# Kernel optimization log

Measured on AMD Instinct MI355X. Metric: run time of the kernel, lower is better.

The kernel has to match this reference:

```python
import jax, jax.numpy as jnp
import numpy as np

SIGMA = 0.01        # config['fscore_sigma']
FSCORE_W = 0.1      # config['fscore_weight']
TASK_W = 1.0        # config['task_weight']
DOMAIN_W = 0.1      # config['domain_weight']


def setup_inputs() -> dict:
    key = jax.random.key(0)
    ks = jax.random.split(key, 11)
    B, N, M, F = 8, 4096, 4096, 512
    H1, H2, D = 256, 128, 6
    return {
        "pred_pc": jax.random.normal(ks[0], (B, N, 3), jnp.float32),
        "target_pc": jax.random.normal(ks[1], (B, M, 3), jnp.float32),
        "domain_features": jax.random.normal(ks[2], (B, F), jnp.float32),
        "dataset_weights": jax.random.uniform(ks[3], (B,), jnp.float32, 0.9, 1.2),
        "W1": jax.random.normal(ks[4], (F, H1), jnp.float32) * 0.02,
        "b1": jnp.zeros((H1,), jnp.float32),
        "W2": jax.random.normal(ks[5], (H1, H2), jnp.float32) * 0.02,
        "b2": jnp.zeros((H2,), jnp.float32),
        "W3": jax.random.normal(ks[6], (H2, D), jnp.float32) * 0.02,
        "b3": jnp.zeros((D,), jnp.float32),
        "domain_labels": jax.random.randint(ks[7], (B,), 0, D),
    }


def _chamfer_mins(pred, tgt):
    # pred: [B,N,3], tgt: [B,M,3] -> squared pairwise dists [B,N,M], then dual mins
    d = (jnp.sum(pred ** 2, axis=2)[:, :, None]
         + jnp.sum(tgt ** 2, axis=2)[:, None, :]
         - 2.0 * jnp.einsum('bnd,bmd->bnm', pred, tgt))
    return jnp.min(d, axis=2), jnp.min(d, axis=1)   # [B,N], [B,M]


def reference(pred_pc, target_pc, domain_features, dataset_weights,
              W1, b1, W2, b2, W3, b3, domain_labels):
    min_a, min_b = _chamfer_mins(pred_pc, target_pc)
    c = 2.0 * SIGMA * SIGMA
    soft_a = jnp.exp(-min_a / c)
    soft_b = jnp.exp(-min_b / c)

    # batch-level task loss (compute_reconstruction_loss on full batch)
    chamfer = jnp.mean(min_a) + jnp.mean(min_b)
    prec = jnp.mean(soft_a)
    rec = jnp.mean(soft_b)
    fscore = 2.0 * prec * rec / (prec + rec + 1e-8)
    task = chamfer + FSCORE_W * (1.0 - fscore)

    # per-sample dataset-weighted loss (vectorized form of the Python loop)
    ch_i = jnp.mean(min_a, axis=1) + jnp.mean(min_b, axis=1)
    p_i = jnp.mean(soft_a, axis=1)
    r_i = jnp.mean(soft_b, axis=1)
    f_i = 2.0 * p_i * r_i / (p_i + r_i + 1e-8)
    loss_i = ch_i + FSCORE_W * (1.0 - f_i)
    dataset_weighted = jnp.mean(dataset_weights * loss_i)

    # domain loss: GRL is identity in forward; classifier in eval mode (dropout off)
    h = jax.nn.relu(domain_features @ W1 + b1)
    h = jax.nn.relu(h @ W2 + b2)
    logits = h @ W3 + b3
    logp = jax.nn.log_softmax(logits, axis=-1)
    domain = -jnp.mean(jnp.take_along_axis(logp, domain_labels[:, None], axis=1))

    total = TASK_W * task + DOMAIN_W * domain + dataset_weighted
    return total
```

## Files before the change

### kernel.cpp

```cpp
#include <hip/hip_runtime.h>
#include <math.h>

#define B 8
#define NPTS 4096
#define QPT 8
#define THREADS 256


template<int S, int LOG2S>
__global__ __launch_bounds__(THREADS, 4) void d1_kernel(
    const float* __restrict__ pred, const float* __restrict__ targ,
    const float* __restrict__ x, const float* __restrict__ W1,
    float* __restrict__ partial, float* __restrict__ sums32,
    float* __restrict__ h1p) {
  constexpr int REFS = NPTS / S;
  int id = blockIdx.x;
  int tid = threadIdx.x;

  __shared__ float4 refs[REFS];
  __shared__ float xs[64];

  if (id < 64) {
    if (id == 0 && tid < 32) sums32[tid] = 0.f;
    int b = id >> 3, kc = id & 7;
    if (tid < 64) xs[tid] = x[b * 512 + kc * 64 + tid];
    __syncthreads();
    float acc = 0.f;
    const float* w = W1 + (size_t)(kc * 64) * 256 + tid;
#pragma unroll 8
    for (int k = 0; k < 64; ++k) acc = fmaf(xs[k], w[k * 256], acc);
    h1p[(b * 8 + kc) * 256 + tid] = acc;
    return;
  }

  int cid = id - 64;
  int split  = cid & (S - 1);
  int qchunk = (cid >> LOG2S) & 1;
  int b      = (cid >> (LOG2S + 1)) & 7;
  int dir    = cid >> (LOG2S + 4);
  const float* qp = dir ? targ : pred;
  const float* rp = dir ? pred : targ;

  const float* rb = rp + ((size_t)b * NPTS + (size_t)split * REFS) * 3;
  for (int i = tid; i < REFS; i += THREADS) {
    float xx = rb[i * 3 + 0], yy = rb[i * 3 + 1], zz = rb[i * 3 + 2];
    refs[i] = make_float4(xx, yy, zz, 0.5f * (xx * xx + yy * yy + zz * zz));
  }
  __syncthreads();

  const float* qb = qp + (size_t)b * NPTS * 3;
  int q0 = qchunk * (QPT * THREADS) + tid;
  float qx[QPT], qy[QPT], qz[QPT], vmin[QPT];
#pragma unroll
  for (int i = 0; i < QPT; ++i) {
    int q = q0 + i * THREADS;
    qx[i] = qb[q * 3 + 0];
    qy[i] = qb[q * 3 + 1];
    qz[i] = qb[q * 3 + 2];
    vmin[i] = 3.4e38f;
  }

  for (int j = 0; j < REFS; j += 8) {
    float4 t[8];
#pragma unroll
    for (int u = 0; u < 8; ++u) t[u] = refs[j + u];
#pragma unroll
    for (int i = 0; i < QPT; ++i) {
      float s[8];
#pragma unroll
      for (int u = 0; u < 8; ++u)
        s[u] = fmaf(-qx[i], t[u].x,
               fmaf(-qy[i], t[u].y, fmaf(-qz[i], t[u].z, t[u].w)));
      float m01 = fminf(s[0], s[1]), m23 = fminf(s[2], s[3]);
      float m45 = fminf(s[4], s[5]), m67 = fminf(s[6], s[7]);
      vmin[i] = fminf(vmin[i],
                      fminf(fminf(m01, m23), fminf(m45, m67)));
    }
  }

  size_t base = (((size_t)dir * B + b) * S + split) * NPTS;
#pragma unroll
  for (int i = 0; i < QPT; ++i) {
    float qn = fmaf(qx[i], qx[i], fmaf(qy[i], qy[i], qz[i] * qz[i]));
    partial[base + q0 + i * THREADS] = fmaf(2.f, vmin[i], qn);
  }
}

template<int S>
__global__ __launch_bounds__(THREADS) void d2_kernel(
    const float* __restrict__ partial, float* __restrict__ sums32,
    const float* __restrict__ h1p, const float* __restrict__ b1,
    const float* __restrict__ W2, float* __restrict__ h2p) {
  int id = blockIdx.x;
  int tid = threadIdx.x;

  if (id >= 256) {
    int lid = id - 256;
    int b = lid >> 1, half = lid & 1;
    __shared__ float hs[128];
    if (tid < 128) {
      int k = half * 128 + tid;
      float a = b1[k];
#pragma unroll
      for (int p = 0; p < 8; ++p) a += h1p[(b * 8 + p) * 256 + k];
      hs[tid] = fmaxf(a, 0.f);
    }
    __syncthreads();
    if (tid < 128) {
      float acc = 0.f;
      const float* w = W2 + (size_t)(half * 128) * 128 + tid;
#pragma unroll 8
      for (int k = 0; k < 128; ++k) acc = fmaf(hs[k], w[k * 128], acc);
      h2p[(b * 2 + half) * 128 + tid] = acc;
    }
    return;
  }

  int chunk = id & 15;
  int b   = (id >> 4) & 7;
  int dir = id >> 7;
  size_t pb = ((size_t)dir * B + b) * S * NPTS;
  int q = chunk * 256 + tid;

  float m = 3.4e38f;
#pragma unroll
  for (int s = 0; s < S; ++s)
    m = fminf(m, partial[pb + (size_t)s * NPTS + q]);
  float s_min = m;
  float s_soft = __expf(-5000.0f * m);

  for (int off = 32; off > 0; off >>= 1) {
    s_min  += __shfl_down(s_min,  off);
    s_soft += __shfl_down(s_soft, off);
  }
  __shared__ float red[8];
  int wave = tid >> 6, lane = tid & 63;
  if (lane == 0) { red[wave * 2] = s_min; red[wave * 2 + 1] = s_soft; }
  __syncthreads();
  if (tid == 0) {
    float a = 0.f, c = 0.f;
    for (int w = 0; w < 4; ++w) { a += red[w * 2]; c += red[w * 2 + 1]; }
    atomicAdd(&sums32[(dir * B + b) * 2 + 0], a);
    atomicAdd(&sums32[(dir * B + b) * 2 + 1], c);
  }
}

__global__ __launch_bounds__(THREADS) void final_kernel(
    const float* __restrict__ h2p, const float* __restrict__ b2,
    const float* __restrict__ W3, const float* __restrict__ b3,
    const int* __restrict__ labels, const float* __restrict__ sums32,
    const float* __restrict__ w, float* __restrict__ out) {
  int tid = threadIdx.x;
  __shared__ float h2s[8 * 128];
  __shared__ float lg[48];
  __shared__ float nlls[8];

  for (int i = tid; i < 1024; i += THREADS) {
    int b = i >> 7, j = i & 127;
    float a = b2[j] + h2p[(b * 2 + 0) * 128 + j] + h2p[(b * 2 + 1) * 128 + j];
    h2s[i] = fmaxf(a, 0.f);
  }
  __syncthreads();
  if (tid < 48) {
    int b = tid / 6, d = tid % 6;
    float acc = b3[d];
#pragma unroll 8
    for (int k = 0; k < 128; ++k) acc = fmaf(h2s[b * 128 + k], W3[k * 6 + d], acc);
    lg[tid] = acc;
  }
  __syncthreads();
  if (tid < 8) {
    int b = tid;
    float mx = lg[b * 6];
    for (int d = 1; d < 6; ++d) mx = fmaxf(mx, lg[b * 6 + d]);
    float se = 0.f;
    for (int d = 0; d < 6; ++d) se += __expf(lg[b * 6 + d] - mx);
    int lab = labels[b];
    nlls[b] = -(lg[b * 6 + lab] - mx - __logf(se));
  }
  __syncthreads();
  if (tid == 0) {
    float chamfer = 0.f, prec = 0.f, rec = 0.f, dsw = 0.f, dom = 0.f;
    for (int b = 0; b < B; ++b) {
      float sa  = sums32[(0 * B + b) * 2 + 0];
      float ssa = sums32[(0 * B + b) * 2 + 1];
      float sb  = sums32[(1 * B + b) * 2 + 0];
      float ssb = sums32[(1 * B + b) * 2 + 1];
      float ma = sa / 4096.f, mb = sb / 4096.f;
      float p = ssa / 4096.f, r = ssb / 4096.f;
      chamfer += ma + mb;
      prec += p; rec += r;
      float f_i = 2.f * p * r / (p + r + 1e-8f);
      float loss_i = ma + mb + 0.1f * (1.f - f_i);
      dsw += w[b] * loss_i;
      dom += nlls[b];
    }
    chamfer *= (1.f / B); prec *= (1.f / B); rec *= (1.f / B);
    dsw *= (1.f / B); dom *= (1.f / B);
    float fscore = 2.f * prec * rec / (prec + rec + 1e-8f);
    float task = chamfer + 0.1f * (1.f - fscore);
    out[0] = 1.0f * task + 0.1f * dom + dsw;
  }
}

template<int S, int LOG2S>
static void run_pipeline(const float* pred, const float* targ, const float* x,
                         const float* wgt, const float* W1, const float* b1,
                         const float* W2, const float* b2, const float* W3,
                         const float* b3, const int* labels, float* out,
                         char* ws, hipStream_t stream) {
  float* partial = (float*)ws;
  float* sums32  = partial + (size_t)2 * B * S * NPTS;
  float* h1p     = sums32 + 32;
  float* h2p     = h1p + 64 * 256;

  hipLaunchKernelGGL((d1_kernel<S, LOG2S>), dim3(64 + 32 * S), dim3(THREADS),
                     0, stream, pred, targ, x, W1, partial, sums32, h1p);
  hipLaunchKernelGGL((d2_kernel<S>), dim3(256 + 16), dim3(THREADS), 0, stream,
                     partial, sums32, h1p, b1, W2, h2p);
  hipLaunchKernelGGL(final_kernel, dim3(1), dim3(THREADS), 0, stream,
                     h2p, b2, W3, b3, labels, sums32, wgt, out);
}

extern "C" void kernel_launch(void* const* d_in, const int* in_sizes, int n_in,
                              void* d_out, int out_size, void* d_ws, size_t ws_size,
                              hipStream_t stream) {
  const float* pred   = (const float*)d_in[0];
  const float* targ   = (const float*)d_in[1];
  const float* x      = (const float*)d_in[2];
  const float* wgt    = (const float*)d_in[3];
  const float* W1     = (const float*)d_in[4];
  const float* b1     = (const float*)d_in[5];
  const float* W2     = (const float*)d_in[6];
  const float* b2     = (const float*)d_in[7];
  const float* W3     = (const float*)d_in[8];
  const float* b3     = (const float*)d_in[9];
  const int*   labels = (const int*)d_in[10];
  float* out = (float*)d_out;
  char* ws = (char*)d_ws;

  auto need = [](int S) {
    return ((size_t)2 * B * S * NPTS + 32 + 64 * 256 + 16 * 128) * sizeof(float);
  };
  if (ws_size >= need(32))
    run_pipeline<32, 5>(pred, targ, x, wgt, W1, b1, W2, b2, W3, b3, labels,
                        out, ws, stream);
  else if (ws_size >= need(16))
    run_pipeline<16, 4>(pred, targ, x, wgt, W1, b1, W2, b2, W3, b3, labels,
                        out, ws, stream);
  else
    run_pipeline<8, 3>(pred, targ, x, wgt, W1, b1, W2, b2, W3, b3, labels,
                       out, ws, stream);
}
```

Measured before the change: 112.6 us.

## Fuse chamfer reduction and MLP tail into one kernel via last-block atomics

```diff
diff --git a/kernel.cpp b/kernel.cpp
--- a/kernel.cpp
+++ b/kernel.cpp
@@ -7,200 +7,224 @@
 #define THREADS 256
 
 
+__device__ __forceinline__ void final_combine(
+    const float* sums32, const float* nlls, const float* w, float* out) {
+  float chamfer = 0.f, prec = 0.f, rec = 0.f, dsw = 0.f, dom = 0.f;
+  for (int b = 0; b < B; ++b) {
+    float sa  = sums32[(0 * B + b) * 2 + 0];
+    float ssa = sums32[(0 * B + b) * 2 + 1];
+    float sb  = sums32[(1 * B + b) * 2 + 0];
+    float ssb = sums32[(1 * B + b) * 2 + 1];
+    float ma = sa / 4096.f, mb = sb / 4096.f;
+    float p = ssa / 4096.f, r = ssb / 4096.f;
+    chamfer += ma + mb;
+    prec += p; rec += r;
+    float f_i = 2.f * p * r / (p + r + 1e-8f);
+    float loss_i = ma + mb + 0.1f * (1.f - f_i);
+    dsw += w[b] * loss_i;
+    dom += nlls[b];
+  }
+  chamfer *= (1.f / B); prec *= (1.f / B); rec *= (1.f / B);
+  dsw *= (1.f / B); dom *= (1.f / B);
+  float fscore = 2.f * prec * rec / (prec + rec + 1e-8f);
+  float task = chamfer + 0.1f * (1.f - fscore);
+  out[0] = 1.0f * task + 0.1f * dom + dsw;
+}
+
+__global__ __launch_bounds__(THREADS) void k_init_l1(
+    const float* __restrict__ x, const float* __restrict__ W1,
+    float* __restrict__ h1p, float* __restrict__ sums32,
+    unsigned int* __restrict__ cnt) {
+  int id = blockIdx.x, tid = threadIdx.x;
+  if (id == 0) {
+    if (tid < 32) sums32[tid] = 0.f;
+    if (tid < 33) cnt[tid] = 0u;
+  }
+  int b = id >> 3, kc = id & 7;
+  __shared__ float xs[64];
+  if (tid < 64) xs[tid] = x[b * 512 + kc * 64 + tid];
+  __syncthreads();
+  float acc = 0.f;
+  const float* w = W1 + (size_t)(kc * 64) * 256 + tid;
+#pragma unroll 8
+  for (int k = 0; k < 64; ++k) acc = fmaf(xs[k], w[k * 256], acc);
+  h1p[(b * 8 + kc) * 256 + tid] = acc;
+}
+
 template<int S, int LOG2S>
-__global__ __launch_bounds__(THREADS, 4) void d1_kernel(
+__global__ __launch_bounds__(THREADS, 4) void k_fused(
     const float* __restrict__ pred, const float* __restrict__ targ,
-    const float* __restrict__ x, const float* __restrict__ W1,
+    const float* __restrict__ h1p, const float* __restrict__ b1,
+    const float* __restrict__ W2, const float* __restrict__ b2,
+    const float* __restrict__ W3, const float* __restrict__ b3,
+    const int* __restrict__ labels, const float* __restrict__ wgt,
     float* __restrict__ partial, float* __restrict__ sums32,
-    float* __restrict__ h1p) {
+    float* __restrict__ nlls, unsigned int* __restrict__ cnt,
+    float* __restrict__ out) {
   constexpr int REFS = NPTS / S;
-  int id = blockIdx.x;
-  int tid = threadIdx.x;
-
-  __shared__ float4 refs[REFS];
-  __shared__ float xs[64];
-
-  if (id < 64) {
-    if (id == 0 && tid < 32) sums32[tid] = 0.f;
-    int b = id >> 3, kc = id & 7;
-    if (tid < 64) xs[tid] = x[b * 512 + kc * 64 + tid];
-    __syncthreads();
-    float acc = 0.f;
-    const float* w = W1 + (size_t)(kc * 64) * 256 + tid;
-#pragma unroll 8
-    for (int k = 0; k < 64; ++k) acc = fmaf(xs[k], w[k * 256], acc);
-    h1p[(b * 8 + kc) * 256 + tid] = acc;
+  int id = blockIdx.x, tid = threadIdx.x;
+
+  __shared__ float4 sbuf4[1040];
+  float* sbuf = (float*)sbuf4;
+  __shared__ unsigned int sflag;
+
+  if (id < 32 * S) {
+    int cid = id;
+    int split  = cid & (S - 1);
+    int qchunk = (cid >> LOG2S) & 1;
+    int b      = (cid >> (LOG2S + 1)) & 7;
+    int dir    = cid >> (LOG2S + 4);
+    const float* qp = dir ? targ : pred;
+    const float* rp = dir ? pred : targ;
+
+    float4* refs = sbuf4;
+    const float* rb = rp + ((size_t)b * NPTS + (size_t)split * REFS) * 3;
+    for (int i = tid; i < REFS; i += THREADS) {
+      float xx = rb[i * 3 + 0], yy = rb[i * 3 + 1], zz = rb[i * 3 + 2];
+      refs[i] = make_float4(xx, yy, zz, 0.5f * (xx * xx + yy * yy + zz * zz));
+    }
+    __syncthreads();
+
+    const float* qb = qp + (size_t)b * NPTS * 3;
+    int q0 = qchunk * (QPT * THREADS) + tid;
+    float qx[QPT], qy[QPT], qz[QPT], vmin[QPT];
+#pragma unroll
+    for (int i = 0; i < QPT; ++i) {
+      int q = q0 + i * THREADS;
+      qx[i] = qb[q * 3 + 0];
+      qy[i] = qb[q * 3 + 1];
+      qz[i] = qb[q * 3 + 2];
+      vmin[i] = 3.4e38f;
+    }
+
+    for (int j = 0; j < REFS; j += 4) {
+      float4 t0 = refs[j + 0], t1 = refs[j + 1];
+      float4 t2 = refs[j + 2], t3 = refs[j + 3];
+      asm volatile("" : "+v"(t0.x), "+v"(t0.y), "+v"(t0.z), "+v"(t0.w),
+                        "+v"(t1.x), "+v"(t1.y), "+v"(t1.z), "+v"(t1.w),
+                        "+v"(t2.x), "+v"(t2.y), "+v"(t2.z), "+v"(t2.w),
+                        "+v"(t3.x), "+v"(t3.y), "+v"(t3.z), "+v"(t3.w));
+#pragma unroll
+      for (int i = 0; i < QPT; ++i) {
+        float s0 = fmaf(-qx[i], t0.x, fmaf(-qy[i], t0.y, fmaf(-qz[i], t0.z, t0.w)));
+        float s1 = fmaf(-qx[i], t1.x, fmaf(-qy[i], t1.y, fmaf(-qz[i], t1.z, t1.w)));
+        float s2 = fmaf(-qx[i], t2.x, fmaf(-qy[i], t2.y, fmaf(-qz[i], t2.z, t2.w)));
+        float s3 = fmaf(-qx[i], t3.x, fmaf(-qy[i], t3.y, fmaf(-qz[i], t3.z, t3.w)));
+        vmin[i] = fminf(fminf(vmin[i], fminf(s0, s1)), fminf(s2, s3));
+      }
+    }
+
+    size_t base = (((size_t)dir * B + b) * S + split) * NPTS;
+#pragma unroll
+    for (int i = 0; i < QPT; ++i) {
+      float qn = fmaf(qx[i], qx[i], fmaf(qy[i], qy[i], qz[i] * qz[i]));
+      partial[base + q0 + i * THREADS] = fmaf(2.f, vmin[i], qn);
+    }
+
+    __threadfence();
+    if (tid == 0) {
+      unsigned int old = atomicAdd(&cnt[(dir * 8 + b) * 2 + qchunk], 1u);
+      sflag = (old == (unsigned int)(S - 1)) ? 1u : 0u;
+    }
+    __syncthreads();
+    if (!sflag) return;
+
+    __threadfence();
+    size_t pb = (size_t)(dir * B + b) * S * NPTS;
+    float s_min = 0.f, s_soft = 0.f;
+#pragma unroll
+    for (int u = 0; u < QPT; ++u) {
+      int q = qchunk * (QPT * THREADS) + u * THREADS + tid;
+      float m = 3.4e38f;
+      for (int s = 0; s < S; ++s)
+        m = fminf(m, partial[pb + (size_t)s * NPTS + q]);
+      s_min  += m;
+      s_soft += __expf(-5000.0f * m);
+    }
+    for (int off = 32; off > 0; off >>= 1) {
+      s_min  += __shfl_down(s_min,  off);
+      s_soft += __shfl_down(s_soft, off);
+    }
+    int wave = tid >> 6, lane = tid & 63;
+    float* red = sbuf + 4160;
+    if (lane == 0) { red[wave * 2] = s_min; red[wave * 2 + 1] = s_soft; }
+    __syncthreads();
+    if (tid == 0) {
+      float a = 0.f, c = 0.f;
+      for (int w = 0; w < 4; ++w) { a += red[w * 2]; c += red[w * 2 + 1]; }
+      atomicAdd(&sums32[(dir * B + b) * 2 + 0], a);
+      atomicAdd(&sums32[(dir * B + b) * 2 + 1], c);
+      __threadfence();
+      unsigned int old = atomicAdd(&cnt[32], 1u);
+      sflag = (old == 32u) ? 1u : 0u;
+    }
+    __syncthreads();
+    if (sflag && tid == 0) { __threadfence(); final_combine(sums32, nlls, wgt, out); }
     return;
   }
 
-  int cid = id - 64;
-  int split  = cid & (S - 1);
-  int qchunk = (cid >> LOG2S) & 1;
-  int b      = (cid >> (LOG2S + 1)) & 7;
-  int dir    = cid >> (LOG2S + 4);
-  const float* qp = dir ? targ : pred;
-  const float* rp = dir ? pred : targ;
-
-  const float* rb = rp + ((size_t)b * NPTS + (size_t)split * REFS) * 3;
-  for (int i = tid; i < REFS; i += THREADS) {
-    float xx = rb[i * 3 + 0], yy = rb[i * 3 + 1], zz = rb[i * 3 + 2];
-    refs[i] = make_float4(xx, yy, zz, 0.5f * (xx * xx + yy * yy + zz * zz));
-  }
-  __syncthreads();
-
-  const float* qb = qp + (size_t)b * NPTS * 3;
-  int q0 = qchunk * (QPT * THREADS) + tid;
-  float qx[QPT], qy[QPT], qz[QPT], vmin[QPT];
-#pragma unroll
-  for (int i = 0; i < QPT; ++i) {
-    int q = q0 + i * THREADS;
-    qx[i] = qb[q * 3 + 0];
-    qy[i] = qb[q * 3 + 1];
-    qz[i] = qb[q * 3 + 2];
-    vmin[i] = 3.4e38f;
-  }
-
-  for (int j = 0; j < REFS; j += 8) {
-    float4 t[8];
-#pragma unroll
-    for (int u = 0; u < 8; ++u) t[u] = refs[j + u];
-#pragma unroll
-    for (int i = 0; i < QPT; ++i) {
-      float s[8];
-#pragma unroll
-      for (int u = 0; u < 8; ++u)
-        s[u] = fmaf(-qx[i], t[u].x,
-               fmaf(-qy[i], t[u].y, fmaf(-qz[i], t[u].z, t[u].w)));
-      float m01 = fminf(s[0], s[1]), m23 = fminf(s[2], s[3]);
-      float m45 = fminf(s[4], s[5]), m67 = fminf(s[6], s[7]);
-      vmin[i] = fminf(vmin[i],
-                      fminf(fminf(m01, m23), fminf(m45, m67)));
-    }
-  }
-
-  size_t base = (((size_t)dir * B + b) * S + split) * NPTS;
-#pragma unroll
-  for (int i = 0; i < QPT; ++i) {
-    float qn = fmaf(qx[i], qx[i], fmaf(qy[i], qy[i], qz[i] * qz[i]));
-    partial[base + q0 + i * THREADS] = fmaf(2.f, vmin[i], qn);
-  }
-}
-
-template<int S>
-__global__ __launch_bounds__(THREADS) void d2_kernel(
-    const float* __restrict__ partial, float* __restrict__ sums32,
-    const float* __restrict__ h1p, const float* __restrict__ b1,
-    const float* __restrict__ W2, float* __restrict__ h2p) {
-  int id = blockIdx.x;
-  int tid = threadIdx.x;
-
-  if (id >= 256) {
-    int lid = id - 256;
-    int b = lid >> 1, half = lid & 1;
-    __shared__ float hs[128];
-    if (tid < 128) {
-      int k = half * 128 + tid;
-      float a = b1[k];
-#pragma unroll
-      for (int p = 0; p < 8; ++p) a += h1p[(b * 8 + p) * 256 + k];
-      hs[tid] = fmaxf(a, 0.f);
-    }
-    __syncthreads();
-    if (tid < 128) {
-      float acc = 0.f;
-      const float* w = W2 + (size_t)(half * 128) * 128 + tid;
-#pragma unroll 8
-      for (int k = 0; k < 128; ++k) acc = fmaf(hs[k], w[k * 128], acc);
-      h2p[(b * 2 + half) * 128 + tid] = acc;
-    }
-    return;
-  }
-
-  int chunk = id & 15;
-  int b   = (id >> 4) & 7;
-  int dir = id >> 7;
-  size_t pb = ((size_t)dir * B + b) * S * NPTS;
-  int q = chunk * 256 + tid;
-
-  float m = 3.4e38f;
-#pragma unroll
-  for (int s = 0; s < S; ++s)
-    m = fminf(m, partial[pb + (size_t)s * NPTS + q]);
-  float s_min = m;
-  float s_soft = __expf(-5000.0f * m);
-
-  for (int off = 32; off > 0; off >>= 1) {
-    s_min  += __shfl_down(s_min,  off);
-    s_soft += __shfl_down(s_soft, off);
-  }
-  __shared__ float red[8];
-  int wave = tid >> 6, lane = tid & 63;
-  if (lane == 0) { red[wave * 2] = s_min; red[wave * 2 + 1] = s_soft; }
-  __syncthreads();
-  if (tid == 0) {
-    float a = 0.f, c = 0.f;
-    for (int w = 0; w < 4; ++w) { a += red[w * 2]; c += red[w * 2 + 1]; }
-    atomicAdd(&sums32[(dir * B + b) * 2 + 0], a);
-    atomicAdd(&sums32[(dir * B + b) * 2 + 1], c);
-  }
-}
-
-__global__ __launch_bounds__(THREADS) void final_kernel(
-    const float* __restrict__ h2p, const float* __restrict__ b2,
-    const float* __restrict__ W3, const float* __restrict__ b3,
-    const int* __restrict__ labels, const float* __restrict__ sums32,
-    const float* __restrict__ w, float* __restrict__ out) {
-  int tid = threadIdx.x;
-  __shared__ float h2s[8 * 128];
-  __shared__ float lg[48];
-  __shared__ float nlls[8];
-
+  float* h1s = sbuf;
+  float* pp  = sbuf + 2048;
+  float* h2s = sbuf;
+  float* lgs = sbuf + 4096;
+
+  for (int i = tid; i < 2048; i += THREADS) {
+    int bb = i >> 8, j = i & 255;
+    float a = b1[j];
+#pragma unroll
+    for (int kc = 0; kc < 8; ++kc) a += h1p[(bb * 8 + kc) * 256 + j];
+    h1s[i] = fmaxf(a, 0.f);
+  }
+  __syncthreads();
+  {
+    int j = tid & 127, half = tid >> 7;
+    float acc[8];
+#pragma unroll
+    for (int bb = 0; bb < 8; ++bb) acc[bb] = 0.f;
+    const float* w = W2 + (size_t)(half * 128) * 128 + j;
+    for (int k = 0; k < 128; ++k) {
+      float wv = w[k * 128];
+      int kk = half * 128 + k;
+#pragma unroll
+      for (int bb = 0; bb < 8; ++bb)
+        acc[bb] = fmaf(h1s[bb * 256 + kk], wv, acc[bb]);
+    }
+    __syncthreads();
+#pragma unroll
+    for (int bb = 0; bb < 8; ++bb) pp[(half * 8 + bb) * 128 + j] = acc[bb];
+  }
+  __syncthreads();
   for (int i = tid; i < 1024; i += THREADS) {
-    int b = i >> 7, j = i & 127;
-    float a = b2[j] + h2p[(b * 2 + 0) * 128 + j] + h2p[(b * 2 + 1) * 128 + j];
+    int bb = i >> 7, j = i & 127;
+    float a = b2[j] + pp[(0 * 8 + bb) * 128 + j] + pp[(1 * 8 + bb) * 128 + j];
     h2s[i] = fmaxf(a, 0.f);
   }
   __syncthreads();
   if (tid < 48) {
-    int b = tid / 6, d = tid % 6;
+    int bb = tid / 6, d = tid % 6;
     float acc = b3[d];
 #pragma unroll 8
-    for (int k = 0; k < 128; ++k) acc = fmaf(h2s[b * 128 + k], W3[k * 6 + d], acc);
-    lg[tid] = acc;
+    for (int k = 0; k < 128; ++k) acc = fmaf(h2s[bb * 128 + k], W3[k * 6 + d], acc);
+    lgs[tid] = acc;
   }
   __syncthreads();
   if (tid < 8) {
-    int b = tid;
-    float mx = lg[b * 6];
-    for (int d = 1; d < 6; ++d) mx = fmaxf(mx, lg[b * 6 + d]);
+    int bb = tid;
+    float mx = lgs[bb * 6];
+    for (int d = 1; d < 6; ++d) mx = fmaxf(mx, lgs[bb * 6 + d]);
     float se = 0.f;
-    for (int d = 0; d < 6; ++d) se += __expf(lg[b * 6 + d] - mx);
-    int lab = labels[b];
-    nlls[b] = -(lg[b * 6 + lab] - mx - __logf(se));
-  }
-  __syncthreads();
+    for (int d = 0; d < 6; ++d) se += __expf(lgs[bb * 6 + d] - mx);
+    int lab = labels[bb];
+    nlls[bb] = -(lgs[bb * 6 + lab] - mx - __logf(se));
+  }
+  __syncthreads();
+  __threadfence();
   if (tid == 0) {
-    float chamfer = 0.f, prec = 0.f, rec = 0.f, dsw = 0.f, dom = 0.f;
-    for (int b = 0; b < B; ++b) {
-      float sa  = sums32[(0 * B + b) * 2 + 0];
-      float ssa = sums32[(0 * B + b) * 2 + 1];
-      float sb  = sums32[(1 * B + b) * 2 + 0];
-      float ssb = sums32[(1 * B + b) * 2 + 1];
-      float ma = sa / 4096.f, mb = sb / 4096.f;
-      float p = ssa / 4096.f, r = ssb / 4096.f;
-      chamfer += ma + mb;
-      prec += p; rec += r;
-      float f_i = 2.f * p * r / (p + r + 1e-8f);
-      float loss_i = ma + mb + 0.1f * (1.f - f_i);
-      dsw += w[b] * loss_i;
-      dom += nlls[b];
-    }
-    chamfer *= (1.f / B); prec *= (1.f / B); rec *= (1.f / B);
-    dsw *= (1.f / B); dom *= (1.f / B);
-    float fscore = 2.f * prec * rec / (prec + rec + 1e-8f);
-    float task = chamfer + 0.1f * (1.f - fscore);
-    out[0] = 1.0f * task + 0.1f * dom + dsw;
-  }
+    unsigned int old = atomicAdd(&cnt[32], 1u);
+    sflag = (old == 32u) ? 1u : 0u;
+  }
+  __syncthreads();
+  if (sflag && tid == 0) { __threadfence(); final_combine(sums32, nlls, wgt, out); }
 }
 
 template<int S, int LOG2S>
@@ -212,14 +236,14 @@
   float* partial = (float*)ws;
   float* sums32  = partial + (size_t)2 * B * S * NPTS;
   float* h1p     = sums32 + 32;
-  float* h2p     = h1p + 64 * 256;
-
-  hipLaunchKernelGGL((d1_kernel<S, LOG2S>), dim3(64 + 32 * S), dim3(THREADS),
-                     0, stream, pred, targ, x, W1, partial, sums32, h1p);
-  hipLaunchKernelGGL((d2_kernel<S>), dim3(256 + 16), dim3(THREADS), 0, stream,
-                     partial, sums32, h1p, b1, W2, h2p);
-  hipLaunchKernelGGL(final_kernel, dim3(1), dim3(THREADS), 0, stream,
-                     h2p, b2, W3, b3, labels, sums32, wgt, out);
+  float* nlls    = h1p + 64 * 256;
+  unsigned int* cnt = (unsigned int*)(nlls + 8);
+
+  hipLaunchKernelGGL(k_init_l1, dim3(64), dim3(THREADS), 0, stream,
+                     x, W1, h1p, sums32, cnt);
+  hipLaunchKernelGGL((k_fused<S, LOG2S>), dim3(32 * S + 1), dim3(THREADS), 0,
+                     stream, pred, targ, h1p, b1, W2, b2, W3, b3, labels, wgt,
+                     partial, sums32, nlls, cnt, out);
 }
 
 extern "C" void kernel_launch(void* const* d_in, const int* in_sizes, int n_in,
@@ -240,15 +264,16 @@
   char* ws = (char*)d_ws;
 
   auto need = [](int S) {
-    return ((size_t)2 * B * S * NPTS + 32 + 64 * 256 + 16 * 128) * sizeof(float);
+    return ((size_t)2 * B * S * NPTS + 32 + 64 * 256 + 8) * sizeof(float)
+           + 33 * sizeof(unsigned int);
   };
-  if (ws_size >= need(32))
+  if (ws_size >= need(64))
+    run_pipeline<64, 6>(pred, targ, x, wgt, W1, b1, W2, b2, W3, b3, labels,
+                        out, ws, stream);
+  else if (ws_size >= need(32))
     run_pipeline<32, 5>(pred, targ, x, wgt, W1, b1, W2, b2, W3, b3, labels,
                         out, ws, stream);
-  else if (ws_size >= need(16))
+  else
     run_pipeline<16, 4>(pred, targ, x, wgt, W1, b1, W2, b2, W3, b3, labels,
                         out, ws, stream);
-  else
-    run_pipeline<8, 3>(pred, targ, x, wgt, W1, b1, W2, b2, W3, b3, labels,
-                       out, ws, stream);
-}
+}
```

Result: slower. 385.2 us (+242.1%).
